# Optimization experiments

Hardware: AMD Instinct MI355X
Metric: run time of the kernel (lower is better)

## Reference

```python
import jax, jax.numpy as jnp
import numpy as np

N_TOKEN = 267735
D_EMBED = 1024
D_PROJ = 1024
DIV_VAL = 4
CUTOFF_ENDS = [0, 20000, 40000, 200000, N_TOKEN]
EMB_SCALE = D_PROJ ** 0.5
INIT_STD = 0.02


def setup_inputs() -> dict:
    key = jax.random.key(0)
    ks = jax.random.split(key, 9)
    inp = jax.random.randint(ks[0], (4, 4096), 0, N_TOKEN, dtype=jnp.int32)
    out = {"inp": inp}
    for i in range(4):
        l, r = CUTOFF_ENDS[i], CUTOFF_ENDS[i + 1]
        d_i = D_EMBED // DIV_VAL ** i  # 1024, 256, 64, 16
        tbl = jax.random.normal(ks[1 + i], (r - l, d_i), dtype=jnp.float32)
        # padding_idx=1: row 1 is zero-initialized in torch nn.Embedding
        tbl = tbl.at[1].set(0.0)
        out[f"emb{i}"] = tbl
        out[f"proj{i}"] = jax.random.normal(ks[5 + i], (D_PROJ, d_i), dtype=jnp.float32) * INIT_STD
    return out


def reference(inp, emb0, emb1, emb2, emb3, proj0, proj1, proj2, proj3):
    tables = [emb0, emb1, emb2, emb3]
    projs = [proj0, proj1, proj2, proj3]
    flat = inp.reshape(-1)                                  # [N]
    out = jnp.zeros((flat.shape[0], D_PROJ), dtype=emb0.dtype)
    for i in range(4):
        l, r = CUTOFF_ENDS[i], CUTOFF_ENDS[i + 1]
        mask = (flat >= l) & (flat < r)                     # [N] bool
        local = jnp.clip(flat - l, 0, r - l - 1)            # in-range local idx
        e_i = tables[i][local]                              # [N, d_i] gather
        p_i = jnp.einsum('nd,pd->np', e_i, projs[i])        # [N, D_PROJ]
        out = out + jnp.where(mask[:, None], p_i, 0.0)      # scatter-by-mask
    out = out * EMB_SCALE
    return out.reshape(*inp.shape, D_PROJ)
```

## Files before the change

kernel.cpp:

```cpp
#include <hip/hip_runtime.h>

#define DPROJ 1024

__global__ void k_zero(int* cnt) {
    if (threadIdx.x < 4) cnt[threadIdx.x] = 0;
}

__global__ void k_classify(const int* __restrict__ inp, int n,
                           int* __restrict__ cnt, int* __restrict__ lists) {
    int t = blockIdx.x * 256 + threadIdx.x;
    if (t >= n) return;
    int v = inp[t];
    int c, l;
    if (v < 20000)       { c = 0; l = v; }
    else if (v < 40000)  { c = 1; l = v - 20000; }
    else if (v < 200000) { c = 2; l = v - 40000; }
    else                 { c = 3; l = v - 200000; }
    unsigned pack = ((unsigned)t << 18) | (unsigned)l;
    int lane = threadIdx.x & 63;
    #pragma unroll
    for (int cc = 0; cc < 4; ++cc) {
        unsigned long long m = __ballot(c == cc);
        if (c == cc) {
            int first = __ffsll(m) - 1;
            int rank  = __popcll(m & ((1ull << lane) - 1ull));
            int base = 0;
            if (lane == first) base = atomicAdd(&cnt[cc], __popcll(m));
            base = __shfl(base, first, 64);
            lists[cc * n + base + rank] = (int)pack;
        }
    }
}

__global__ __launch_bounds__(256, 4) void k_gemm(
    const int* __restrict__ cnt, const int* __restrict__ lists, int n,
    const float* __restrict__ e0, const float* __restrict__ p0,
    const float* __restrict__ e1, const float* __restrict__ p1,
    const float* __restrict__ e2, const float* __restrict__ p2,
    const float* __restrict__ e3, const float* __restrict__ p3,
    float* __restrict__ out)
{
    constexpr int TM = 64, TN = 128, KC = 16, TNP = TN + 4;

    const int z     = blockIdx.z;
    const int count = cnt[z];
    const int row0  = blockIdx.y * TM;
    if (row0 >= count) return;

    const float* emb  = (z == 0) ? e0 : (z == 1) ? e1 : (z == 2) ? e2 : e3;
    const float* proj = (z == 0) ? p0 : (z == 1) ? p1 : (z == 2) ? p2 : p3;
    const int    K    = (z == 0) ? 1024 : (z == 1) ? 256 : (z == 2) ? 64 : 16;
    const int*   list = lists + (long)z * n;
    const int    col0 = blockIdx.x * TN;

    __shared__ int   s_tok[TM];
    __shared__ int   s_loc[TM];
    __shared__ float e_s[TM * KC];
    __shared__ float p_s[KC * TNP];

    const int tid = threadIdx.x;
    if (tid < TM) {
        int r = row0 + tid;
        if (r < count) {
            unsigned pk = (unsigned)list[r];
            s_tok[tid] = (int)(pk >> 18);
            s_loc[tid] = (int)(pk & 0x3FFFFu);
        } else { s_tok[tid] = -1; s_loc[tid] = -1; }
    }
    __syncthreads();

    const int tr = tid >> 5;
    const int tc = tid & 31;

    const int  em   = tid >> 2;
    const int  ekq  = tid & 3;
    const int  eloc = s_loc[em];
    const long ebase = (eloc >= 0) ? (long)eloc * K : 0;
    const bool evalid = (eloc >= 0);

    float acc[8][4];
    #pragma unroll
    for (int i = 0; i < 8; ++i)
        #pragma unroll
        for (int j = 0; j < 4; ++j) acc[i][j] = 0.f;

    for (int kb = 0; kb < K; kb += KC) {
        if (kb) __syncthreads();

        float4 ev4 = make_float4(0.f, 0.f, 0.f, 0.f);
        if (evalid) ev4 = *(const float4*)&emb[ebase + kb + ekq * 4];
        *(float4*)&e_s[em * KC + ekq * 4] = ev4;

        #pragma unroll
        for (int it = 0; it < 2; ++it) {
            int p = (tid >> 2) + it * 64;
            float4 v = *(const float4*)&proj[(long)(col0 + p) * K + kb + ekq * 4];
            p_s[(ekq * 4 + 0) * TNP + p] = v.x;
            p_s[(ekq * 4 + 1) * TNP + p] = v.y;
            p_s[(ekq * 4 + 2) * TNP + p] = v.z;
            p_s[(ekq * 4 + 3) * TNP + p] = v.w;
        }
        __syncthreads();

        #pragma unroll
        for (int k = 0; k < KC; k += 4) {
            float pv[4][4];
            #pragma unroll
            for (int kk = 0; kk < 4; ++kk)
                *(float4*)&pv[kk][0] = *(const float4*)&p_s[(k + kk) * TNP + tc * 4];
            #pragma unroll
            for (int i = 0; i < 8; ++i) {
                float evr[4];
                *(float4*)&evr[0] = *(const float4*)&e_s[(tr * 8 + i) * KC + k];
                #pragma unroll
                for (int kk = 0; kk < 4; ++kk)
                    #pragma unroll
                    for (int j = 0; j < 4; ++j)
                        acc[i][j] = fmaf(evr[kk], pv[kk][j], acc[i][j]);
            }
        }
    }

    #pragma unroll
    for (int i = 0; i < 8; ++i) {
        int tok = s_tok[tr * 8 + i];
        if (tok >= 0) {
            float4 v = make_float4(acc[i][0] * 32.f, acc[i][1] * 32.f,
                                   acc[i][2] * 32.f, acc[i][3] * 32.f);
            *(float4*)&out[(long)tok * DPROJ + col0 + tc * 4] = v;
        }
    }
}

extern "C" void kernel_launch(void* const* d_in, const int* in_sizes, int n_in,
                              void* d_out, int out_size, void* d_ws, size_t ws_size,
                              hipStream_t stream) {
    const int*   inp = (const int*)d_in[0];
    const float* e0  = (const float*)d_in[1];
    const float* p0  = (const float*)d_in[2];
    const float* e1  = (const float*)d_in[3];
    const float* p1  = (const float*)d_in[4];
    const float* e2  = (const float*)d_in[5];
    const float* p2  = (const float*)d_in[6];
    const float* e3  = (const float*)d_in[7];
    const float* p3  = (const float*)d_in[8];
    float* out = (float*)d_out;
    const int n = in_sizes[0];

    int* cnt   = (int*)d_ws;
    int* lists = cnt + 4;

    k_zero<<<1, 64, 0, stream>>>(cnt);
    k_classify<<<(n + 255) / 256, 256, 0, stream>>>(inp, n, cnt, lists);

    dim3 grid(DPROJ / 128, (n + 63) / 64, 4);
    k_gemm<<<grid, 256, 0, stream>>>(cnt, lists, n, e0, p0, e1, p1, e2, p2, e3, p3, out);
}
```

Baseline: 276.6 us.

## Use bf16 MFMA for grouped GEMM and single-block scan classify

```diff
diff --git a/kernel.cpp b/kernel.cpp
--- a/kernel.cpp
+++ b/kernel.cpp
@@ -1,34 +1,67 @@
 #include <hip/hip_runtime.h>
+#include <hip/hip_bf16.h>
 
 #define DPROJ 1024
 
-__global__ void k_zero(int* cnt) {
-    if (threadIdx.x < 4) cnt[threadIdx.x] = 0;
+typedef float  f32x4  __attribute__((ext_vector_type(4)));
+typedef short  bf16x8 __attribute__((ext_vector_type(8)));
+
+__device__ __forceinline__ unsigned pk2(float a, float b) {
+    __hip_bfloat162 h = __float22bfloat162_rn(make_float2(a, b));
+    unsigned r; __builtin_memcpy(&r, &h, 4); return r;
 }
 
-__global__ void k_classify(const int* __restrict__ inp, int n,
-                           int* __restrict__ cnt, int* __restrict__ lists) {
-    int t = blockIdx.x * 256 + threadIdx.x;
-    if (t >= n) return;
-    int v = inp[t];
-    int c, l;
-    if (v < 20000)       { c = 0; l = v; }
-    else if (v < 40000)  { c = 1; l = v - 20000; }
-    else if (v < 200000) { c = 2; l = v - 40000; }
-    else                 { c = 3; l = v - 200000; }
-    unsigned pack = ((unsigned)t << 18) | (unsigned)l;
-    int lane = threadIdx.x & 63;
-    #pragma unroll
-    for (int cc = 0; cc < 4; ++cc) {
-        unsigned long long m = __ballot(c == cc);
-        if (c == cc) {
-            int first = __ffsll(m) - 1;
-            int rank  = __popcll(m & ((1ull << lane) - 1ull));
-            int base = 0;
-            if (lane == first) base = atomicAdd(&cnt[cc], __popcll(m));
-            base = __shfl(base, first, 64);
-            lists[cc * n + base + rank] = (int)pack;
-        }
+__global__ __launch_bounds__(1024) void k_classify(
+    const int* __restrict__ inp, int n,
+    int* __restrict__ cnt, int* __restrict__ lists)
+{
+    __shared__ uint2 s[1024];
+    const int tid = threadIdx.x;
+    const int pt  = (n + 1023) >> 10;
+    const int t0  = tid * pt;
+
+    int v[16];
+    unsigned cp = 0;
+    uint2 mine = make_uint2(0u, 0u);
+    for (int j = 0; j < pt; ++j) {
+        int t = t0 + j, c = 0;
+        if (t < n) {
+            int x = inp[t]; v[j] = x;
+            c = (x >= 20000) + (x >= 40000) + (x >= 200000);
+            if      (c == 0) mine.x += 1u;
+            else if (c == 1) mine.x += 1u << 16;
+            else if (c == 2) mine.y += 1u;
+            else             mine.y += 1u << 16;
+        } else v[j] = 0;
+        cp |= (unsigned)c << (2 * j);
+    }
+    s[tid] = mine;
+    for (int off = 1; off < 1024; off <<= 1) {
+        __syncthreads();
+        uint2 add = make_uint2(0u, 0u);
+        if (tid >= off) add = s[tid - off];
+        __syncthreads();
+        s[tid].x += add.x; s[tid].y += add.y;
+    }
+    __syncthreads();
+    uint2 tot = s[1023];
+    uint2 inc = s[tid];
+    unsigned run[4] = { (inc.x & 0xffffu) - (mine.x & 0xffffu),
+                        (inc.x >> 16)     - (mine.x >> 16),
+                        (inc.y & 0xffffu) - (mine.y & 0xffffu),
+                        (inc.y >> 16)     - (mine.y >> 16) };
+    if (tid == 0) {
+        cnt[0] = (int)(tot.x & 0xffffu); cnt[1] = (int)(tot.x >> 16);
+        cnt[2] = (int)(tot.y & 0xffffu); cnt[3] = (int)(tot.y >> 16);
+    }
+    const int cut[4] = {0, 20000, 40000, 200000};
+    for (int j = 0; j < pt; ++j) {
+        int t = t0 + j;
+        if (t >= n) break;
+        int c = (int)((cp >> (2 * j)) & 3u);
+        int l = v[j] - cut[c];
+        unsigned pos = run[c]++;
+        lists[c * n + (int)pos] = (int)(((unsigned)t << 18) | (unsigned)l);
     }
 }
 
@@ -40,7 +73,7 @@
     const float* __restrict__ e3, const float* __restrict__ p3,
     float* __restrict__ out)
 {
-    constexpr int TM = 64, TN = 128, KC = 16, TNP = TN + 4;
+    constexpr int TM = 64, TN = 128, KC = 32, STR = 40;
 
     const int z     = blockIdx.z;
     const int count = cnt[z];
@@ -50,13 +83,13 @@
     const float* emb  = (z == 0) ? e0 : (z == 1) ? e1 : (z == 2) ? e2 : e3;
     const float* proj = (z == 0) ? p0 : (z == 1) ? p1 : (z == 2) ? p2 : p3;
     const int    K    = (z == 0) ? 1024 : (z == 1) ? 256 : (z == 2) ? 64 : 16;
-    const int*   list = lists + (long)z * n;
+    const int*   list = lists + (size_t)z * n;
     const int    col0 = blockIdx.x * TN;
 
     __shared__ int   s_tok[TM];
     __shared__ int   s_loc[TM];
-    __shared__ float e_s[TM * KC];
-    __shared__ float p_s[KC * TNP];
+    __shared__ short e_s[TM * STR];
+    __shared__ short p_s[TN * STR];
 
     const int tid = threadIdx.x;
     if (tid < TM) {
@@ -69,65 +102,71 @@
     }
     __syncthreads();
 
-    const int tr = tid >> 5;
-    const int tc = tid & 31;
+    const int  erow = tid >> 2, egrp = tid & 3;
+    const int  eloc = s_loc[erow];
+    const bool ev   = (eloc >= 0);
+    const size_t ebase = ev ? (size_t)eloc * K : 0;
 
-    const int  em   = tid >> 2;
-    const int  ekq  = tid & 3;
-    const int  eloc = s_loc[em];
-    const long ebase = (eloc >= 0) ? (long)eloc * K : 0;
-    const bool evalid = (eloc >= 0);
+    const int wave = tid >> 6, lane = tid & 63;
+    const int lm = lane & 15, quad = lane >> 4;
 
-    float acc[8][4];
+    f32x4 acc[8];
     #pragma unroll
-    for (int i = 0; i < 8; ++i)
-        #pragma unroll
-        for (int j = 0; j < 4; ++j) acc[i][j] = 0.f;
+    for (int i = 0; i < 8; ++i) acc[i] = (f32x4){0.f, 0.f, 0.f, 0.f};
 
     for (int kb = 0; kb < K; kb += KC) {
         if (kb) __syncthreads();
 
-        float4 ev4 = make_float4(0.f, 0.f, 0.f, 0.f);
-        if (evalid) ev4 = *(const float4*)&emb[ebase + kb + ekq * 4];
-        *(float4*)&e_s[em * KC + ekq * 4] = ev4;
-
+        {
+            float f[8] = {0.f, 0.f, 0.f, 0.f, 0.f, 0.f, 0.f, 0.f};
+            int ko = kb + egrp * 8;
+            if (ev && ko < K) {
+                float4 a = *(const float4*)&emb[ebase + ko];
+                float4 b = *(const float4*)&emb[ebase + ko + 4];
+                f[0] = a.x; f[1] = a.y; f[2] = a.z; f[3] = a.w;
+                f[4] = b.x; f[5] = b.y; f[6] = b.z; f[7] = b.w;
+            }
+            uint4 q; q.x = pk2(f[0], f[1]); q.y = pk2(f[2], f[3]);
+                     q.z = pk2(f[4], f[5]); q.w = pk2(f[6], f[7]);
+            *(uint4*)&e_s[erow * STR + egrp * 8] = q;
+        }
         #pragma unroll
         for (int it = 0; it < 2; ++it) {
-            int p = (tid >> 2) + it * 64;
-            float4 v = *(const float4*)&proj[(long)(col0 + p) * K + kb + ekq * 4];
-            p_s[(ekq * 4 + 0) * TNP + p] = v.x;
-            p_s[(ekq * 4 + 1) * TNP + p] = v.y;
-            p_s[(ekq * 4 + 2) * TNP + p] = v.z;
-            p_s[(ekq * 4 + 3) * TNP + p] = v.w;
+            int u    = tid + it * 256;
+            int prow = u >> 2, pgrp = u & 3;
+            int ko   = kb + pgrp * 8;
+            float f[8] = {0.f, 0.f, 0.f, 0.f, 0.f, 0.f, 0.f, 0.f};
+            if (ko < K) {
+                const float* src = &proj[(size_t)(col0 + prow) * K + ko];
+                float4 a = *(const float4*)src;
+                float4 b = *(const float4*)(src + 4);
+                f[0] = a.x; f[1] = a.y; f[2] = a.z; f[3] = a.w;
+                f[4] = b.x; f[5] = b.y; f[6] = b.z; f[7] = b.w;
+            }
+            uint4 q; q.x = pk2(f[0], f[1]); q.y = pk2(f[2], f[3]);
+                     q.z = pk2(f[4], f[5]); q.w = pk2(f[6], f[7]);
+            *(uint4*)&p_s[prow * STR + pgrp * 8] = q;
         }
         __syncthreads();
 
+        bf16x8 af = *(const bf16x8*)&e_s[(wave * 16 + lm) * STR + quad * 8];
         #pragma unroll
-        for (int k = 0; k < KC; k += 4) {
-            float pv[4][4];
-            #pragma unroll
-            for (int kk = 0; kk < 4; ++kk)
-                *(float4*)&pv[kk][0] = *(const float4*)&p_s[(k + kk) * TNP + tc * 4];
-            #pragma unroll
-            for (int i = 0; i < 8; ++i) {
-                float evr[4];
-                *(float4*)&evr[0] = *(const float4*)&e_s[(tr * 8 + i) * KC + k];
-                #pragma unroll
-                for (int kk = 0; kk < 4; ++kk)
-                    #pragma unroll
-                    for (int j = 0; j < 4; ++j)
-                        acc[i][j] = fmaf(evr[kk], pv[kk][j], acc[i][j]);
-            }
+        for (int ns = 0; ns < 8; ++ns) {
+            bf16x8 bf = *(const bf16x8*)&p_s[(ns * 16 + lm) * STR + quad * 8];
+            acc[ns] = __builtin_amdgcn_mfma_f32_16x16x32_bf16(af, bf, acc[ns], 0, 0, 0);
         }
     }
 
+    int toks[4];
     #pragma unroll
-    for (int i = 0; i < 8; ++i) {
-        int tok = s_tok[tr * 8 + i];
-        if (tok >= 0) {
-            float4 v = make_float4(acc[i][0] * 32.f, acc[i][1] * 32.f,
-                                   acc[i][2] * 32.f, acc[i][3] * 32.f);
-            *(float4*)&out[(long)tok * DPROJ + col0 + tc * 4] = v;
+    for (int r = 0; r < 4; ++r) toks[r] = s_tok[wave * 16 + quad * 4 + r];
+    #pragma unroll
+    for (int ns = 0; ns < 8; ++ns) {
+        int col = col0 + ns * 16 + lm;
+        #pragma unroll
+        for (int r = 0; r < 4; ++r) {
+            if (toks[r] >= 0)
+                out[(size_t)toks[r] * DPROJ + col] = acc[ns][r] * 32.f;
         }
     }
 }
@@ -150,8 +189,7 @@
     int* cnt   = (int*)d_ws;
     int* lists = cnt + 4;
 
-    k_zero<<<1, 64, 0, stream>>>(cnt);
-    k_classify<<<(n + 255) / 256, 256, 0, stream>>>(inp, n, cnt, lists);
+    k_classify<<<1, 1024, 0, stream>>>(inp, n, cnt, lists);
 
     dim3 grid(DPROJ / 128, (n + 63) / 64, 4);
     k_gemm<<<grid, 256, 0, stream>>>(cnt, lists, n, e0, p0, e1, p1, e2, p2, e3, p3, out);
```

Result: faster. 262.5 us (-5.1%).
